# Kernel tuning notes

Measured on AMD Instinct MI355X. Metric: run time of the kernel, lower is better.

The kernel has to match this reference:

```python
import jax, jax.numpy as jnp
import numpy as np

EMB = 768
HEADS = 8
HEAD_DIM = EMB // HEADS  # 96


def setup_inputs() -> dict:
    key = jax.random.key(0)
    ks = jax.random.split(key, 5)
    B, N = 4, 2048
    x = jax.random.normal(ks[0], (B, N, EMB), dtype=jnp.float32)
    s_in = 1.0 / np.sqrt(EMB)
    # weights stored as (in, out); equivalent to torch Linear y = x @ W + b
    w_qkv = jax.random.normal(ks[1], (EMB, 3 * EMB), dtype=jnp.float32) * s_in
    b_qkv = jax.random.normal(ks[2], (3 * EMB,), dtype=jnp.float32) * 0.02
    w_proj = jax.random.normal(ks[3], (EMB, EMB), dtype=jnp.float32) * s_in
    b_proj = jax.random.normal(ks[4], (EMB,), dtype=jnp.float32) * 0.02
    return {"x": x, "w_qkv": w_qkv, "b_qkv": b_qkv, "w_proj": w_proj, "b_proj": b_proj}


def reference(x, w_qkv, b_qkv, w_proj, b_proj):
    B, N, _ = x.shape
    qkv = x @ w_qkv + b_qkv  # [B, N, 3*EMB]
    # rearrange 'b n (h d qkv) -> qkv b h n d': qkv is the innermost split axis
    qkv = qkv.reshape(B, N, HEADS, HEAD_DIM, 3)
    qkv = jnp.transpose(qkv, (4, 0, 2, 1, 3))  # [3, B, H, N, D]
    q, k, v = qkv[0], qkv[1], qkv[2]
    inv_scale = 1.0 / np.sqrt(HEAD_DIM)  # applied AFTER softmax (faithful to source)
    scores = jnp.einsum('bhqd,bhkd->bhqk', q, k)
    attn = jax.nn.softmax(scores, axis=-1) * inv_scale
    out = jnp.einsum('bhqk,bhkd->bhqd', attn, v)
    out = jnp.transpose(out, (0, 2, 1, 3)).reshape(B, N, EMB)  # b h n d -> b n (h d)
    return out @ w_proj + b_proj
```

## Files before the change

### kernel.cpp

```cpp
#include <hip/hip_runtime.h>
#include <hip/hip_bf16.h>

#define EMB 768
#define NHEADS 8
#define HDIM 96
#define SEQ 2048
#define BATCH 4
#define QKV_COLS 2304
#define PB ((size_t)SEQ * EMB)

typedef _Float16 f16;
typedef _Float16 f16x8 __attribute__((ext_vector_type(8)));
typedef float f32x4 __attribute__((ext_vector_type(4)));

__device__ __forceinline__ void gl_lds16(const f16* g, f16* l) {
  __builtin_amdgcn_global_load_lds((const __attribute__((address_space(1))) void*)g,
                                   (__attribute__((address_space(3))) void*)l, 16, 0, 0);
}
__device__ __forceinline__ f32x4 shflx4(f32x4 v, int m) {
  f32x4 r;
  r[0] = __shfl_xor(v[0], m); r[1] = __shfl_xor(v[1], m);
  r[2] = __shfl_xor(v[2], m); r[3] = __shfl_xor(v[3], m);
  return r;
}
__device__ __forceinline__ f32x4 vmax4(f32x4 a, f32x4 b) {
  f32x4 r;
  r[0] = fmaxf(a[0], b[0]); r[1] = fmaxf(a[1], b[1]);
  r[2] = fmaxf(a[2], b[2]); r[3] = fmaxf(a[3], b[3]);
  return r;
}

__global__ __launch_bounds__(256) void conv_x8_k(const float* __restrict__ in, size_t in_off,
                                                 f16* __restrict__ out, int n8) {
  int i = blockIdx.x * 256 + threadIdx.x;
  if (i >= n8) return;
  const float4 a = *(const float4*)(in + in_off + (size_t)i * 8);
  const float4 b = *(const float4*)(in + in_off + (size_t)i * 8 + 4);
  f16x8 o;
  o[0] = (f16)a.x; o[1] = (f16)a.y; o[2] = (f16)a.z; o[3] = (f16)a.w;
  o[4] = (f16)b.x; o[5] = (f16)b.y; o[6] = (f16)b.z; o[7] = (f16)b.w;
  *(f16x8*)(out + (size_t)i * 8) = o;
}

__global__ __launch_bounds__(256) void pre_k(
    const float* __restrict__ wq, f16* __restrict__ wqT,
    const float* __restrict__ wp, f16* __restrict__ wpT,
    const float* __restrict__ bq_in, float* __restrict__ bq_out,
    const float* __restrict__ bp_in, float* __restrict__ bp_out)
{
  __shared__ float t[32][33];
  const int bid = blockIdx.x;
  const int tx = threadIdx.x & 31, ty = threadIdx.x >> 5;
  if (bid < 1728 + 576) {
    const float* in; f16* out; int C, ct, rt; bool qkv;
    if (bid < 1728) { in = wq; out = wqT; C = QKV_COLS;
                      ct = (bid % 72) * 32; rt = (bid / 72) * 32; qkv = true; }
    else            { const int b2 = bid - 1728; in = wp; out = wpT; C = EMB;
                      ct = (b2 % 24) * 32; rt = (b2 / 24) * 32; qkv = false; }
#pragma unroll
    for (int p = 0; p < 4; p++)
      t[p * 8 + ty][tx] = in[(size_t)(rt + p * 8 + ty) * C + ct + tx];
    __syncthreads();
#pragma unroll
    for (int p = 0; p < 4; p++) {
      const int c = ct + p * 8 + ty;
      int colp;
      if (qkv) { const int h = c / 288, rem = c - h * 288, d = rem / 3, s = rem - d * 3;
                 colp = s * 768 + h * 96 + d; }
      else     colp = c;
      out[(size_t)colp * EMB + rt + tx] = (f16)t[tx][p * 8 + ty];
    }
  } else {
    for (int i = threadIdx.x; i < QKV_COLS; i += 256) {
      const int s = i / 768, rem = i - s * 768, h = rem / 96, d = rem - h * 96;
      bq_out[i] = bq_in[h * 288 + d * 3 + s];
    }
    for (int i = threadIdx.x; i < EMB; i += 256) bp_out[i] = bp_in[i];
  }
}

template<int MODE>
__global__ __launch_bounds__(256) void gemm_bt(
    const f16* __restrict__ A, const f16* __restrict__ Bt,
    const float* __restrict__ bias, float* __restrict__ Cout,
    f16* __restrict__ QK, f16* __restrict__ Vt,
    int M, int N, int Kd)
{
  __shared__ f16 smem[MODE == 1 ? 17408 : 8192];
  f16* sA = smem;
  f16* sB = smem + 4096;
  const int tid  = threadIdx.x;
  const int wave = tid >> 6, lane = tid & 63;
  const int quad = lane >> 4, l16 = lane & 15;
  int lin = blockIdx.y * gridDim.x + blockIdx.x;
  {
    const int nwg = gridDim.x * gridDim.y;
    if ((nwg & 7) == 0) {
      const int chunk = nwg >> 3;
      lin = (lin & 7) * chunk + (lin >> 3);
    }
  }
  const int tile_m = (lin / gridDim.x) * 128, tile_n = (lin % gridDim.x) * 128;
  const int wm = (wave >> 1) * 64, wn = (wave & 1) * 64;

  f32x4 acc[4][4];
  for (int i = 0; i < 4; i++)
    for (int j = 0; j < 4; j++)
      acc[i][j] = f32x4{0.f, 0.f, 0.f, 0.f};

  for (int k0 = 0; k0 < Kd; k0 += 32) {
    __syncthreads();
#pragma unroll
    for (int it = 0; it < 2; it++) {
      const int ch  = (it * 4 + wave) * 64 + lane;
      const int row = ch >> 2, c8 = (ch & 3) * 8;
      if (MODE == 2) {
        const int grow = tile_m + row;
        const int bb = grow >> 11, n = grow & 2047;
        const int hh = k0 / 96, d0 = k0 - hh * 96 + c8;
        gl_lds16(A + ((size_t)(bb * NHEADS + hh) * SEQ + n) * HDIM + d0,
                 &sA[(it * 4 + wave) * 512]);
      } else {
        gl_lds16(A + (size_t)(tile_m + row) * Kd + k0 + c8, &sA[(it * 4 + wave) * 512]);
      }
      gl_lds16(Bt + (size_t)(tile_n + row) * Kd + k0 + c8, &sB[(it * 4 + wave) * 512]);
    }
    __syncthreads();

    f16x8 af[4], bfr[4];
    for (int i = 0; i < 4; i++) af[i]  = *(const f16x8*)&sA[(wm + i * 16 + l16) * 32 + quad * 8];
    for (int j = 0; j < 4; j++) bfr[j] = *(const f16x8*)&sB[(wn + j * 16 + l16) * 32 + quad * 8];
    for (int i = 0; i < 4; i++)
      for (int j = 0; j < 4; j++)
        acc[i][j] = __builtin_amdgcn_mfma_f32_16x16x32_f16(af[i], bfr[j], acc[i][j], 0, 0, 0);
  }

  if (MODE == 1 && tile_n >= 1536) {
    __syncthreads();
    f16* sT = smem;
    for (int j = 0; j < 4; j++) {
      const int cl = wn + j * 16 + l16;
      const float bv = bias[tile_n + cl];
      for (int i = 0; i < 4; i++)
        for (int r = 0; r < 4; r++)
          sT[cl * 136 + wm + i * 16 + quad * 4 + r] = (f16)(acc[i][j][r] + bv);
    }
    __syncthreads();
    const int bb = tile_m >> 11;
    const int n0 = tile_m & 2047;
#pragma unroll
    for (int l = 0; l < 8; l++) {
      const int cc = l * 256 + tid;
      const int rh = cc >> 4, nof = (cc & 15) * 8;
      const int hd = (tile_n - 1536) + rh;
      const int h = hd / 96, d = hd - h * 96;
      f16x8 v = *(const f16x8*)&sT[rh * 136 + nof];
      *(f16x8*)(Vt + ((size_t)(bb * NHEADS + h) * HDIM + d) * SEQ + n0 + nof) = v;
    }
  } else {
    for (int j = 0; j < 4; j++) {
      const int col = tile_n + wn + j * 16 + l16;
      const float bv = bias[col];
      for (int i = 0; i < 4; i++) {
        for (int r = 0; r < 4; r++) {
          const int row = tile_m + wm + i * 16 + quad * 4 + r;
          const float fv = acc[i][j][r] + bv;
          if (MODE != 1) Cout[(size_t)row * N + col] = fv;
          else           QK  [(size_t)row * 1536 + col] = (f16)fv;
        }
      }
    }
  }
}

__global__ __launch_bounds__(256, 2) void attn_k(
    const f16* __restrict__ QK, const f16* __restrict__ Vt,
    f16* __restrict__ Out , int nbh)
{
  __shared__ f16 sK[128 * 96];
  __shared__ f16 sV[96 * 128];
  __shared__ f16 sP[128 * 64];
  const int tid  = threadIdx.x;
  const int wave = tid >> 6, lane = tid & 63;
  const int quad = lane >> 4, l16 = lane & 15;

  const int bid = blockIdx.x;
  const int xcd = bid & 7, idx = bid >> 3;
  const int bh  = xcd * (nbh >> 3) + (idx >> 4);
  const int qt  = idx & 15;
  const int b = bh >> 3, h = bh & 7;

  const int wrow = wave * 32;

  const f16* Qb = QK + (size_t)(b * SEQ + qt * 128 + wrow) * 1536 + h * 96;
  const f16* Kb = QK + (size_t)(b * SEQ) * 1536 + 768 + h * 96;
  const f16* Vb = Vt + (size_t)bh * HDIM * SEQ;

  int koff[6], voff[6];
#pragma unroll
  for (int i = 0; i < 6; i++) {
    const int ck = i * 256 + tid;
    const int krow = ck / 12, pu = ck - krow * 12;
    const int u = (pu + 12 - krow % 12) % 12;
    koff[i] = krow * 1536 + u * 8;
    const int vd = ck >> 4, pv = ck & 15;
    voff[i] = vd * SEQ + (pv ^ (vd & 15)) * 8;
  }

  f16x8 qf[2][3];
#pragma unroll
  for (int ti = 0; ti < 2; ti++)
#pragma unroll
    for (int kc = 0; kc < 3; kc++)
      qf[ti][kc] = *(const f16x8*)(Qb + (size_t)(ti * 16 + l16) * 1536 + kc * 32 + quad * 8);

  f32x4 oacc[2][6];
#pragma unroll
  for (int ti = 0; ti < 2; ti++)
#pragma unroll
    for (int dj = 0; dj < 6; dj++)
      oacc[ti][dj] = f32x4{0.f, 0.f, 0.f, 0.f};
  f32x4 m_run[2], l_run[2];
#pragma unroll
  for (int ti = 0; ti < 2; ti++) {
    m_run[ti] = f32x4{-1e30f, -1e30f, -1e30f, -1e30f};
    l_run[ti] = f32x4{0.f, 0.f, 0.f, 0.f};
  }

  {
#pragma unroll
    for (int i = 0; i < 6; i++) gl_lds16(Kb + koff[i], &sK[(i * 256 + wave * 64) * 8]);
#pragma unroll
    for (int i = 0; i < 6; i++) gl_lds16(Vb + voff[i], &sV[(i * 256 + wave * 64) * 8]);
  }

  const int NT = SEQ / 128;
  for (int kt = 0; kt < NT; kt++) {
    if (kt == 0) asm volatile("s_waitcnt vmcnt(0)" ::: "memory");
    else         asm volatile("s_waitcnt vmcnt(6)" ::: "memory");
    __builtin_amdgcn_s_barrier();
    __builtin_amdgcn_sched_barrier(0);

    f32x4 sacc[2][8];
#pragma unroll
    for (int ti = 0; ti < 2; ti++)
#pragma unroll
      for (int j = 0; j < 8; j++)
        sacc[ti][j] = f32x4{0.f, 0.f, 0.f, 0.f};
#pragma unroll
    for (int kc = 0; kc < 3; kc++) {
#pragma unroll
      for (int j = 0; j < 8; j++) {
        const int krow = j * 16 + l16;
        const f16x8 kf = *(const f16x8*)&sK[krow * 96 + ((kc * 4 + quad + krow) % 12) * 8];
        sacc[0][j] = __builtin_amdgcn_mfma_f32_16x16x32_f16(qf[0][kc], kf, sacc[0][j], 0, 0, 0);
        sacc[1][j] = __builtin_amdgcn_mfma_f32_16x16x32_f16(qf[1][kc], kf, sacc[1][j], 0, 0, 0);
      }
    }

    __builtin_amdgcn_sched_barrier(0);
    __builtin_amdgcn_s_barrier();
    if (kt < NT - 1) {
      const f16* kb = Kb + (size_t)((kt + 1) * 128) * 1536;
#pragma unroll
      for (int i = 0; i < 6; i++) gl_lds16(kb + koff[i], &sK[(i * 256 + wave * 64) * 8]);
    }
    __builtin_amdgcn_sched_barrier(0);

    f32x4 rsv[2];
#pragma unroll
    for (int ti = 0; ti < 2; ti++) {
      f32x4 vmx = sacc[ti][0];
#pragma unroll
      for (int j = 1; j < 8; j++) vmx = vmax4(vmx, sacc[ti][j]);
      const int ok = __all(vmx[0] <= m_run[ti][0] + 8.f &&
                           vmx[1] <= m_run[ti][1] + 8.f &&
                           vmx[2] <= m_run[ti][2] + 8.f &&
                           vmx[3] <= m_run[ti][3] + 8.f);
      if (!ok) {
        for (int m = 1; m < 16; m <<= 1) vmx = vmax4(vmx, shflx4(vmx, m));
        const f32x4 nm = vmax4(m_run[ti], vmx);
        f32x4 alpha;
        alpha[0] = __expf(m_run[ti][0] - nm[0]); alpha[1] = __expf(m_run[ti][1] - nm[1]);
        alpha[2] = __expf(m_run[ti][2] - nm[2]); alpha[3] = __expf(m_run[ti][3] - nm[3]);
        m_run[ti] = nm;
        l_run[ti] *= alpha;
#pragma unroll
        for (int dj = 0; dj < 6; dj++) oacc[ti][dj] *= alpha;
      }
      rsv[ti] = f32x4{0.f, 0.f, 0.f, 0.f};
    }

    if (kt < NT - 1) asm volatile("s_waitcnt vmcnt(6)" ::: "memory");
    else             asm volatile("s_waitcnt vmcnt(0)" ::: "memory");
    __builtin_amdgcn_s_barrier();
    __builtin_amdgcn_sched_barrier(0);

#pragma unroll
    for (int c2 = 0; c2 < 2; c2++) {
#pragma unroll
      for (int ti = 0; ti < 2; ti++) {
        const int prow = wrow + ti * 16 + quad * 4;
#pragma unroll
        for (int jl = 0; jl < 4; jl++) {
          const int j = c2 * 4 + jl;
          f32x4 p;
          p[0] = __expf(sacc[ti][j][0] - m_run[ti][0]);
          p[1] = __expf(sacc[ti][j][1] - m_run[ti][1]);
          p[2] = __expf(sacc[ti][j][2] - m_run[ti][2]);
          p[3] = __expf(sacc[ti][j][3] - m_run[ti][3]);
          rsv[ti] += p;
          const int unit = jl * 2 + (l16 >> 3);
          const int within = l16 & 7;
#pragma unroll
          for (int rr = 0; rr < 4; rr++) {
            const int row = prow + rr;
            sP[row * 64 + (unit ^ (row & 7)) * 8 + within] = (f16)p[rr];
          }
        }
      }
#pragma unroll
      for (int kc2 = 0; kc2 < 2; kc2++) {
        const f16x8 pf0 = *(const f16x8*)&sP[(wrow + l16) * 64
                                            + ((kc2 * 4 + quad) ^ (l16 & 7)) * 8];
        const f16x8 pf1 = *(const f16x8*)&sP[(wrow + 16 + l16) * 64
                                            + ((kc2 * 4 + quad) ^ (l16 & 7)) * 8];
#pragma unroll
        for (int dj = 0; dj < 6; dj++) {
          const int vph = (c2 * 8 + kc2 * 4 + quad) ^ l16;
          const f16x8 vf = *(const f16x8*)&sV[(dj * 16 + l16) * 128 + vph * 8];
          oacc[0][dj] = __builtin_amdgcn_mfma_f32_16x16x32_f16(pf0, vf, oacc[0][dj], 0, 0, 0);
          oacc[1][dj] = __builtin_amdgcn_mfma_f32_16x16x32_f16(pf1, vf, oacc[1][dj], 0, 0, 0);
        }
      }
    }

    __builtin_amdgcn_sched_barrier(0);
    __builtin_amdgcn_s_barrier();
    if (kt < NT - 1) {
      const f16* vb = Vb + (kt + 1) * 128;
#pragma unroll
      for (int i = 0; i < 6; i++) gl_lds16(vb + voff[i], &sV[(i * 256 + wave * 64) * 8]);
    }
    __builtin_amdgcn_sched_barrier(0);

#pragma unroll
    for (int ti = 0; ti < 2; ti++) l_run[ti] += rsv[ti];
  }

#pragma unroll
  for (int ti = 0; ti < 2; ti++)
    for (int m = 1; m < 16; m <<= 1) l_run[ti] += shflx4(l_run[ti], m);

  const float inv_scale = 0.10206207261596577f;
#pragma unroll
  for (int ti = 0; ti < 2; ti++) {
#pragma unroll
    for (int r = 0; r < 4; r++) {
      const int qrow = qt * 128 + wrow + ti * 16 + quad * 4 + r;
      const float invl = inv_scale / l_run[ti][r];
      const size_t base = ((size_t)bh * SEQ + qrow) * HDIM;
#pragma unroll
      for (int dj = 0; dj < 6; dj++)
        Out[base + dj * 16 + l16] = (f16)(oacc[ti][dj][r] * invl);
    }
  }
}

extern "C" void kernel_launch(void* const* d_in, const int* in_sizes, int n_in,
                              void* d_out, int out_size, void* d_ws, size_t ws_size,
                              hipStream_t stream) {
  const float* x      = (const float*)d_in[0];
  const float* w_qkv  = (const float*)d_in[1];
  const float* b_qkv  = (const float*)d_in[2];
  const float* w_proj = (const float*)d_in[3];
  const float* b_proj = (const float*)d_in[4];
  float* outF = (float*)d_out;

  const size_t fixed = 256 + (size_t)QKV_COLS * EMB * 2 + (size_t)EMB * EMB * 2
                     + QKV_COLS * 4 + EMB * 4 + 256;
  const size_t perb = (size_t)4 * PB * 2;
  int nb = (ws_size >= fixed + 4 * perb) ? 4 : (ws_size >= fixed + 2 * perb) ? 2 : 1;

  char* ws = (char*)d_ws;
  ws += 256;
  f16*   wqkvT  = (f16*)ws;   ws += (size_t)QKV_COLS * EMB * 2;
  f16*   wprojT = (f16*)ws;   ws += (size_t)EMB * EMB * 2;
  float* bq     = (float*)ws; ws += (size_t)QKV_COLS * 4;
  float* bp     = (float*)ws; ws += (size_t)EMB * 4 + 256;
  f16* QK   = (f16*)ws;       ws += (size_t)nb * 2 * PB * 2;
  f16* Vt   = (f16*)ws;       ws += (size_t)nb * PB * 2;
  f16* attn = (f16*)ws;       ws += (size_t)nb * PB * 2;

  pre_k<<<1728 + 576 + 1, 256, 0, stream>>>(w_qkv, wqkvT, w_proj, wprojT,
                                            b_qkv, bq, b_proj, bp);

  for (int outer = 0; outer < BATCH / nb; outer++) {
    const int bbase = outer * nb;
    const size_t goff = (size_t)bbase * PB;
    f16* xg = (f16*)(outF + goff);
    const int n8 = (int)((size_t)nb * PB / 8);
    conv_x8_k<<<(n8 + 255) / 256, 256, 0, stream>>>(x, goff, xg, n8);

    dim3 g1(QKV_COLS / 128, nb * SEQ / 128);
    gemm_bt<1><<<g1, 256, 0, stream>>>(xg, wqkvT, bq, nullptr, QK, Vt,
                                       nb * SEQ, QKV_COLS, EMB);

    attn_k<<<dim3(16 * nb * NHEADS), 256, 0, stream>>>(QK, Vt, attn, nb * NHEADS);

    dim3 g3(EMB / 128, nb * SEQ / 128);
    gemm_bt<2><<<g3, 256, 0, stream>>>(attn, wprojT, bp, outF + goff,
                                       nullptr, nullptr,
                                       nb * SEQ, EMB, EMB);
  }
}
```

Baseline: 290.4 us.

## Split attention KV range in two halves with a separate merge kernel

Each attention block now covers half of the key sequence, which doubles the grid, and a new merge kernel combines the two partial outputs using the stored per-row max and sum. K/V tiles shrink to 64 keys, the P buffer reuses the K shared memory, and K and V are loaded together after each step with a full vmcnt(0) wait. The goal is more parallelism and occupancy from smaller LDS use, but the change gives up the previous overlap of loads with compute and adds an extra kernel plus extra global traffic for the partial outputs.

Result: faster. 278.8 us (-4.0%).

```diff
diff --git a/kernel.cpp b/kernel.cpp
--- a/kernel.cpp
+++ b/kernel.cpp
@@ -175,36 +175,40 @@
 
 __global__ __launch_bounds__(256, 2) void attn_k(
     const f16* __restrict__ QK, const f16* __restrict__ Vt,
-    f16* __restrict__ Out , int nbh)
+    f16* __restrict__ oh0, f16* __restrict__ oh1, float* __restrict__ ml,
+    int nbh)
 {
-  __shared__ f16 sK[128 * 96];
-  __shared__ f16 sV[96 * 128];
-  __shared__ f16 sP[128 * 64];
+  __shared__ f16 sK[64 * 96];
+  __shared__ f16 sV[96 * 64];
+  f16* sP = sK;
   const int tid  = threadIdx.x;
   const int wave = tid >> 6, lane = tid & 63;
   const int quad = lane >> 4, l16 = lane & 15;
 
   const int bid = blockIdx.x;
   const int xcd = bid & 7, idx = bid >> 3;
-  const int bh  = xcd * (nbh >> 3) + (idx >> 4);
-  const int qt  = idx & 15;
+  const int bh  = xcd * (nbh >> 3) + (idx >> 5);
+  const int rem = idx & 31;
+  const int qt  = rem & 15, half = rem >> 4;
   const int b = bh >> 3, h = bh & 7;
+  const int nrows = nbh * SEQ;
 
   const int wrow = wave * 32;
 
   const f16* Qb = QK + (size_t)(b * SEQ + qt * 128 + wrow) * 1536 + h * 96;
-  const f16* Kb = QK + (size_t)(b * SEQ) * 1536 + 768 + h * 96;
-  const f16* Vb = Vt + (size_t)bh * HDIM * SEQ;
-
-  int koff[6], voff[6];
-#pragma unroll
-  for (int i = 0; i < 6; i++) {
+  const f16* Kb = QK + (size_t)(b * SEQ) * 1536 + 768 + h * 96
+                + (size_t)(half * 1024) * 1536;
+  const f16* Vb = Vt + (size_t)bh * HDIM * SEQ + half * 1024;
+
+  int koff[3], voff[3];
+#pragma unroll
+  for (int i = 0; i < 3; i++) {
     const int ck = i * 256 + tid;
     const int krow = ck / 12, pu = ck - krow * 12;
     const int u = (pu + 12 - krow % 12) % 12;
     koff[i] = krow * 1536 + u * 8;
-    const int vd = ck >> 4, pv = ck & 15;
-    voff[i] = vd * SEQ + (pv ^ (vd & 15)) * 8;
+    const int vd = ck >> 3, pv = ck & 7;
+    voff[i] = vd * SEQ + (pv ^ (vd & 7)) * 8;
   }
 
   f16x8 qf[2][3];
@@ -227,30 +231,26 @@
     l_run[ti] = f32x4{0.f, 0.f, 0.f, 0.f};
   }
 
-  {
-#pragma unroll
-    for (int i = 0; i < 6; i++) gl_lds16(Kb + koff[i], &sK[(i * 256 + wave * 64) * 8]);
-#pragma unroll
-    for (int i = 0; i < 6; i++) gl_lds16(Vb + voff[i], &sV[(i * 256 + wave * 64) * 8]);
-  }
-
-  const int NT = SEQ / 128;
-  for (int kt = 0; kt < NT; kt++) {
-    if (kt == 0) asm volatile("s_waitcnt vmcnt(0)" ::: "memory");
-    else         asm volatile("s_waitcnt vmcnt(6)" ::: "memory");
+#pragma unroll
+  for (int i = 0; i < 3; i++) gl_lds16(Kb + koff[i], &sK[(i * 256 + wave * 64) * 8]);
+#pragma unroll
+  for (int i = 0; i < 3; i++) gl_lds16(Vb + voff[i], &sV[(i * 256 + wave * 64) * 8]);
+
+  for (int it = 0; it < 16; it++) {
+    asm volatile("s_waitcnt vmcnt(0)" ::: "memory");
     __builtin_amdgcn_s_barrier();
     __builtin_amdgcn_sched_barrier(0);
 
-    f32x4 sacc[2][8];
+    f32x4 sacc[2][4];
 #pragma unroll
     for (int ti = 0; ti < 2; ti++)
 #pragma unroll
-      for (int j = 0; j < 8; j++)
+      for (int j = 0; j < 4; j++)
         sacc[ti][j] = f32x4{0.f, 0.f, 0.f, 0.f};
 #pragma unroll
     for (int kc = 0; kc < 3; kc++) {
 #pragma unroll
-      for (int j = 0; j < 8; j++) {
+      for (int j = 0; j < 4; j++) {
         const int krow = j * 16 + l16;
         const f16x8 kf = *(const f16x8*)&sK[krow * 96 + ((kc * 4 + quad + krow) % 12) * 8];
         sacc[0][j] = __builtin_amdgcn_mfma_f32_16x16x32_f16(qf[0][kc], kf, sacc[0][j], 0, 0, 0);
@@ -260,11 +260,6 @@
 
     __builtin_amdgcn_sched_barrier(0);
     __builtin_amdgcn_s_barrier();
-    if (kt < NT - 1) {
-      const f16* kb = Kb + (size_t)((kt + 1) * 128) * 1536;
-#pragma unroll
-      for (int i = 0; i < 6; i++) gl_lds16(kb + koff[i], &sK[(i * 256 + wave * 64) * 8]);
-    }
     __builtin_amdgcn_sched_barrier(0);
 
     f32x4 rsv[2];
@@ -272,7 +267,7 @@
     for (int ti = 0; ti < 2; ti++) {
       f32x4 vmx = sacc[ti][0];
 #pragma unroll
-      for (int j = 1; j < 8; j++) vmx = vmax4(vmx, sacc[ti][j]);
+      for (int j = 1; j < 4; j++) vmx = vmax4(vmx, sacc[ti][j]);
       const int ok = __all(vmx[0] <= m_run[ti][0] + 8.f &&
                            vmx[1] <= m_run[ti][1] + 8.f &&
                            vmx[2] <= m_run[ti][2] + 8.f &&
@@ -291,19 +286,14 @@
       rsv[ti] = f32x4{0.f, 0.f, 0.f, 0.f};
     }
 
-    if (kt < NT - 1) asm volatile("s_waitcnt vmcnt(6)" ::: "memory");
-    else             asm volatile("s_waitcnt vmcnt(0)" ::: "memory");
-    __builtin_amdgcn_s_barrier();
-    __builtin_amdgcn_sched_barrier(0);
-
 #pragma unroll
     for (int c2 = 0; c2 < 2; c2++) {
 #pragma unroll
       for (int ti = 0; ti < 2; ti++) {
         const int prow = wrow + ti * 16 + quad * 4;
 #pragma unroll
-        for (int jl = 0; jl < 4; jl++) {
-          const int j = c2 * 4 + jl;
+        for (int jl = 0; jl < 2; jl++) {
+          const int j = c2 * 2 + jl;
           f32x4 p;
           p[0] = __expf(sacc[ti][j][0] - m_run[ti][0]);
           p[1] = __expf(sacc[ti][j][1] - m_run[ti][1]);
@@ -315,32 +305,32 @@
 #pragma unroll
           for (int rr = 0; rr < 4; rr++) {
             const int row = prow + rr;
-            sP[row * 64 + (unit ^ (row & 7)) * 8 + within] = (f16)p[rr];
+            sP[row * 32 + (unit ^ (row & 3)) * 8 + within] = (f16)p[rr];
           }
         }
       }
 #pragma unroll
-      for (int kc2 = 0; kc2 < 2; kc2++) {
-        const f16x8 pf0 = *(const f16x8*)&sP[(wrow + l16) * 64
-                                            + ((kc2 * 4 + quad) ^ (l16 & 7)) * 8];
-        const f16x8 pf1 = *(const f16x8*)&sP[(wrow + 16 + l16) * 64
-                                            + ((kc2 * 4 + quad) ^ (l16 & 7)) * 8];
+      for (int ti = 0; ti < 2; ti++) {
+        const int prw = wrow + ti * 16 + l16;
+        const f16x8 pf = *(const f16x8*)&sP[prw * 32 + (quad ^ (l16 & 3)) * 8];
 #pragma unroll
         for (int dj = 0; dj < 6; dj++) {
-          const int vph = (c2 * 8 + kc2 * 4 + quad) ^ l16;
-          const f16x8 vf = *(const f16x8*)&sV[(dj * 16 + l16) * 128 + vph * 8];
-          oacc[0][dj] = __builtin_amdgcn_mfma_f32_16x16x32_f16(pf0, vf, oacc[0][dj], 0, 0, 0);
-          oacc[1][dj] = __builtin_amdgcn_mfma_f32_16x16x32_f16(pf1, vf, oacc[1][dj], 0, 0, 0);
+          const int vph = (c2 * 4 + quad) ^ (l16 & 7);
+          const f16x8 vf = *(const f16x8*)&sV[(dj * 16 + l16) * 64 + vph * 8];
+          oacc[ti][dj] = __builtin_amdgcn_mfma_f32_16x16x32_f16(pf, vf, oacc[ti][dj], 0, 0, 0);
         }
       }
     }
 
     __builtin_amdgcn_sched_barrier(0);
     __builtin_amdgcn_s_barrier();
-    if (kt < NT - 1) {
-      const f16* vb = Vb + (kt + 1) * 128;
-#pragma unroll
-      for (int i = 0; i < 6; i++) gl_lds16(vb + voff[i], &sV[(i * 256 + wave * 64) * 8]);
+    if (it < 15) {
+      const f16* kb = Kb + (size_t)((it + 1) * 64) * 1536;
+      const f16* vb = Vb + (it + 1) * 64;
+#pragma unroll
+      for (int i = 0; i < 3; i++) gl_lds16(kb + koff[i], &sK[(i * 256 + wave * 64) * 8]);
+#pragma unroll
+      for (int i = 0; i < 3; i++) gl_lds16(vb + voff[i], &sV[(i * 256 + wave * 64) * 8]);
     }
     __builtin_amdgcn_sched_barrier(0);
 
@@ -352,19 +342,45 @@
   for (int ti = 0; ti < 2; ti++)
     for (int m = 1; m < 16; m <<= 1) l_run[ti] += shflx4(l_run[ti], m);
 
-  const float inv_scale = 0.10206207261596577f;
+  f16* oh = half ? oh1 : oh0;
 #pragma unroll
   for (int ti = 0; ti < 2; ti++) {
 #pragma unroll
     for (int r = 0; r < 4; r++) {
       const int qrow = qt * 128 + wrow + ti * 16 + quad * 4 + r;
-      const float invl = inv_scale / l_run[ti][r];
-      const size_t base = ((size_t)bh * SEQ + qrow) * HDIM;
+      const float invl = 1.f / l_run[ti][r];
+      const size_t rowg = (size_t)bh * SEQ + qrow;
 #pragma unroll
       for (int dj = 0; dj < 6; dj++)
-        Out[base + dj * 16 + l16] = (f16)(oacc[ti][dj][r] * invl);
-    }
-  }
+        oh[rowg * 96 + dj * 16 + l16] = (f16)(oacc[ti][dj][r] * invl);
+      if (l16 == 0) {
+        ml[((size_t)half * nrows + rowg) * 2 + 0] = m_run[ti][r];
+        ml[((size_t)half * nrows + rowg) * 2 + 1] = l_run[ti][r];
+      }
+    }
+  }
+}
+
+__global__ __launch_bounds__(256) void merge_k(
+    const f16* __restrict__ oh0_, const f16* __restrict__ oh1,
+    const float* __restrict__ ml, f16* __restrict__ out,
+    int nchunks, int nrows)
+{
+  const int t = blockIdx.x * 256 + threadIdx.x;
+  if (t >= nchunks) return;
+  const int row = t / 12, off = (t - row * 12) * 8;
+  const float m0 = ml[(size_t)row * 2 + 0], l0 = ml[(size_t)row * 2 + 1];
+  const float m1 = ml[((size_t)nrows + row) * 2 + 0], l1 = ml[((size_t)nrows + row) * 2 + 1];
+  const float nm = fmaxf(m0, m1);
+  const float w0 = __expf(m0 - nm) * l0, w1 = __expf(m1 - nm) * l1;
+  const float s = 0.10206207261596577f / (w0 + w1);
+  const f16x8 a = *(const f16x8*)(oh0_ + (size_t)row * 96 + off);
+  const f16x8 bvv = *(const f16x8*)(oh1 + (size_t)row * 96 + off);
+  f16x8 o;
+#pragma unroll
+  for (int j = 0; j < 8; j++)
+    o[j] = (f16)((w0 * (float)a[j] + w1 * (float)bvv[j]) * s);
+  *(f16x8*)(out + (size_t)row * 96 + off) = o;
 }
 
 extern "C" void kernel_launch(void* const* d_in, const int* in_sizes, int n_in,
@@ -398,7 +414,11 @@
   for (int outer = 0; outer < BATCH / nb; outer++) {
     const int bbase = outer * nb;
     const size_t goff = (size_t)bbase * PB;
+    const int nbh = nb * NHEADS;
+    const int nrows = nbh * SEQ;
     f16* xg = (f16*)(outF + goff);
+    f16* oh1 = (f16*)(outF + goff);
+    float* ml = (float*)((char*)(outF + goff) + (size_t)nb * PB * 2);
     const int n8 = (int)((size_t)nb * PB / 8);
     conv_x8_k<<<(n8 + 255) / 256, 256, 0, stream>>>(x, goff, xg, n8);
 
@@ -406,7 +426,11 @@
     gemm_bt<1><<<g1, 256, 0, stream>>>(xg, wqkvT, bq, nullptr, QK, Vt,
                                        nb * SEQ, QKV_COLS, EMB);
 
-    attn_k<<<dim3(16 * nb * NHEADS), 256, 0, stream>>>(QK, Vt, attn, nb * NHEADS);
+    attn_k<<<dim3(32 * nbh), 256, 0, stream>>>(QK, Vt, attn, oh1, ml, nbh);
+
+    const int nchunks = nrows * 12;
+    merge_k<<<(nchunks + 255) / 256, 256, 0, stream>>>(attn, oh1, ml, attn,
+                                                       nchunks, nrows);
 
     dim3 g3(EMB / 128, nb * SEQ / 128);
     gemm_bt<2><<<g3, 256, 0, stream>>>(attn, wprojT, bp, outF + goff,
```
